# Kernel tuning notes

Measured on AMD Instinct MI355X. Metric: run time of the kernel, lower is better.

## Reference

```python
import jax, jax.numpy as jnp
import numpy as np

N = 6144
IN_F = 256
OUT_F = 64
ALPHA = 0.2  # leaky relu slope
NEG_INF = -9e15
ADJ_DENSITY = 0.01


def setup_inputs() -> dict:
    key = jax.random.key(0)
    kx, ka, kw, kat, ks, ke = jax.random.split(key, 6)
    x = jax.random.normal(kx, (N, IN_F), dtype=jnp.float32)
    adj = (jax.random.uniform(ka, (N, N)) < ADJ_DENSITY).astype(jnp.float32)
    adj = adj.at[jnp.arange(N), jnp.arange(N)].set(0.0)
    # xavier-uniform-ish init scale (gain 1.414)
    def xavier(k, shape):
        fan_in, fan_out = shape[0], shape[1]
        lim = 1.414 * np.sqrt(6.0 / (fan_in + fan_out))
        return jax.random.uniform(k, shape, minval=-lim, maxval=lim, dtype=jnp.float32)
    W = xavier(kw, (IN_F, OUT_F))
    a = xavier(kat, (2 * OUT_F, 1))
    W_si = xavier(ks, (1, 1))
    W_ei = xavier(ke, (1, 1))
    return {"x": x, "adj": adj, "W": W, "a": a, "W_si": W_si, "W_ei": W_ei}


def reference(x, adj, W, a, W_si, W_ei):
    # h: [N, F_out]
    h = x @ W
    # additive GAT score: e[i,j] = leakyrelu(Wh1[i] + Wh2[j])
    Wh1 = h @ a[:OUT_F, :]           # [N, 1]
    Wh2 = h @ a[OUT_F:, :]           # [N, 1]
    e = jax.nn.leaky_relu(Wh1 + Wh2.T, negative_slope=ALPHA)  # [N, N]
    # adjacency-power topology bias
    adj2 = adj @ adj
    adj3 = adj2 @ adj
    adj_w = adj + adj2 + adj3
    adj_w = adj_w.at[jnp.arange(N), jnp.arange(N)].set(0.0)
    e = jnp.abs(W_ei) * e + jnp.abs(W_si) * adj_w
    # masked softmax over neighbors (row-wise)
    scores = jnp.where(adj > 0, e, NEG_INF)
    attention = jax.nn.softmax(scores, axis=1)
    # dropout omitted (eval mode / training=False)
    h_prime = attention @ h
    return jax.nn.elu(h_prime)
```

## Files before the change

kernel.cpp:

```cpp
#include <hip/hip_runtime.h>
#include <math.h>

#define N 6144
#define MAXD 128
#define NWORDS 96
#define NW32 192

typedef unsigned long long u64;
typedef unsigned int u32;
typedef unsigned char u8;
typedef float f4 __attribute__((ext_vector_type(4)));


__device__ __forceinline__ int a_addr(int j) {
    int vdx = (j & ~255) | ((j & 3) << 6) | ((j >> 2) & 63);
    return (((vdx >> 2) & 7) << 10) | ((vdx >> 5) << 2) | (vdx & 3);
}

#define FA(s, c, a, b, ci) { u32 _t = (a) ^ (b); (s) = _t ^ (ci); (c) = ((a) & (b)) | ((ci) & _t); }

template <int START>
__device__ __forceinline__ void badd_from(u32* p, u32 cy) {
    #pragma unroll
    for (int q = START; q < 6; ++q) { u32 x = p[q] & cy; p[q] ^= cy; cy = x; }
    p[6] ^= cy;
}

__device__ __forceinline__ void csa15(u32* p, const u32* x) {
    u32 s0,c0,s1,c1,s2,c2,s3,c3,s4,c4;
    FA(s0,c0, x[0], x[1], x[2]);
    FA(s1,c1, x[3], x[4], x[5]);
    FA(s2,c2, x[6], x[7], x[8]);
    FA(s3,c3, x[9], x[10], x[11]);
    FA(s4,c4, x[12], x[13], x[14]);
    u32 t0,d0,u0,d1;
    FA(t0,d0, s0, s1, s2);
    FA(u0,d1, s3, s4, t0);
    u32 e0,f0,e1,f1,e2,f2;
    FA(e0,f0, c0, c1, c2);
    FA(e1,f1, c3, c4, d0);
    FA(e2,f2, e0, e1, d1);
    u32 g0,h0;
    FA(g0,h0, f0, f1, f2);
    badd_from<0>(p, u0);
    badd_from<1>(p, e2);
    badd_from<2>(p, g0);
    badd_from<3>(p, h0);
}

__global__ __launch_bounds__(256) void k_gemm_h(
    const float* __restrict__ x, const float* __restrict__ W,
    const float* __restrict__ a,
    float* __restrict__ h, float* __restrict__ Wh1, float* __restrict__ Wh2,
    int* __restrict__ col_cnt)
{
    int gid = blockIdx.x * 256 + threadIdx.x;
    if (gid < N) col_cnt[gid] = 0;

    __shared__ float Wl[256 * 64];
    int t = threadIdx.x;
    #pragma unroll
    for (int c = 0; c < 64; ++c) Wl[c * 256 + t] = W[c * 256 + t];
    __syncthreads();

    int w = t >> 6, lane = t & 63;
    int i0 = blockIdx.x * 32 + w * 8;
    const float* xr = x + (long)i0 * 256;

    float acc[8] = {0.f, 0.f, 0.f, 0.f, 0.f, 0.f, 0.f, 0.f};
    for (int k0 = 0; k0 < 256; k0 += 4) {
        float4 xv[8];
        #pragma unroll
        for (int r = 0; r < 8; ++r)
            xv[r] = *(const float4*)(xr + (long)r * 256 + k0);
        #pragma unroll
        for (int kk = 0; kk < 4; ++kk) {
            float wv = Wl[(k0 + kk) * 64 + lane];
            #pragma unroll
            for (int r = 0; r < 8; ++r) {
                float xs = (kk == 0) ? xv[r].x : (kk == 1) ? xv[r].y
                         : (kk == 2) ? xv[r].z : xv[r].w;
                acc[r] = fmaf(xs, wv, acc[r]);
            }
        }
    }

    #pragma unroll
    for (int r = 0; r < 8; ++r) {
        int i = i0 + r;
        h[(long)i * 64 + lane] = acc[r];
        float s1 = acc[r] * a[lane];
        float s2 = acc[r] * a[64 + lane];
        #pragma unroll
        for (int off = 32; off; off >>= 1) {
            s1 += __shfl_xor(s1, off, 64);
            s2 += __shfl_xor(s2, off, 64);
        }
        if (lane == 0) { Wh1[i] = s1; Wh2[i] = s2; }
    }
}

__global__ __launch_bounds__(256) void k_build(
    const float* __restrict__ adj,
    u64* __restrict__ rowbits, int* __restrict__ row_cnt, int* __restrict__ row_list,
    int* __restrict__ col_cnt, int* __restrict__ col_list)
{
    int i = blockIdx.x;
    int t = threadIdx.x, w = t >> 6, lane = t & 63;
    __shared__ int cnt;
    if (t == 0) cnt = 0;
    __syncthreads();

    const f4* ar = (const f4*)(adj + (long)i * N) + (w * 6) * 64;

    f4 v[6];
    #pragma unroll
    for (int c = 0; c < 6; ++c)
        v[c] = __builtin_nontemporal_load(ar + c * 64 + lane);

    u64 m[6][4];
    #pragma unroll
    for (int c = 0; c < 6; ++c) {
        m[c][0] = __ballot(v[c].x != 0.0f);
        m[c][1] = __ballot(v[c].y != 0.0f);
        m[c][2] = __ballot(v[c].z != 0.0f);
        m[c][3] = __ballot(v[c].w != 0.0f);
    }

    int tot = 0;
    #pragma unroll
    for (int c = 0; c < 6; ++c) {
        #pragma unroll
        for (int p = 0; p < 4; ++p) tot += __popcll(m[c][p]);
    }
    int base = 0;
    if (lane == 0 && tot) base = atomicAdd(&cnt, tot);
    base = __shfl(base, 0, 64);

    u64* rb = rowbits + (long)i * NWORDS + w * 24;
    #pragma unroll
    for (int c = 0; c < 6; ++c) {
        #pragma unroll
        for (int p = 0; p < 4; ++p) {
            u64 mm = m[c][p];
            if (lane == 0) rb[c * 4 + p] = mm;
            if ((mm >> lane) & 1ull) {
                int rank = __popcll(mm & ((1ull << lane) - 1ull));
                int s = base + rank;
                int j = (w * 6 + c) * 256 + (lane << 2) + p;
                if (s < MAXD) row_list[(long)i * MAXD + s] = j;
                int sc = atomicAdd(&col_cnt[j], 1);
                if (sc < MAXD) col_list[(long)j * MAXD + sc] = i;
            }
            base += __popcll(mm);
        }
    }
    __syncthreads();
    if (t == 0) row_cnt[i] = cnt < 127 ? cnt : 127;
}

__global__ __launch_bounds__(192) void k_attn(
    const float* __restrict__ h, const float* __restrict__ Wh1, const float* __restrict__ Wh2,
    const u64* __restrict__ rowbits,
    const int* __restrict__ row_cnt, const int* __restrict__ row_list,
    const int* __restrict__ col_cnt, const int* __restrict__ col_list,
    const float* __restrict__ W_si, const float* __restrict__ W_ei,
    float* __restrict__ out)
{
    __shared__ u32 adj2p[8 * 256];
    __shared__ int nbr[MAXD];
    __shared__ int ccbuf[MAXD];
    __shared__ float lrbuf[MAXD];
    __shared__ float ebuf[MAXD];
    __shared__ float part[192];
    __shared__ float sh_max, sh_sum;

    int i = blockIdx.x;
    int t = threadIdx.x, w = t >> 6, lane = t & 63;
    int deg = row_cnt[i];
    deg = deg < 127 ? deg : 127;

    if (deg == 0) {
        float acc = 0.f;
        for (int r = w; r < N; r += 3) acc += h[(long)r * 64 + lane];
        part[t] = acc;
        __syncthreads();
        if (w == 0) {
            float s = part[lane] + part[64 + lane] + part[128 + lane];
            s *= (1.0f / N);
            out[(long)i * 64 + lane] = s > 0.f ? s : expm1f(s);
        }
        return;
    }

    float aWei = fabsf(W_ei[0]);
    float aWsi = fabsf(W_si[0]);

    if (t < deg) {
        int j = row_list[(long)i * MAXD + t];
        nbr[t] = j;
        int cc = col_cnt[j];
        ccbuf[t] = cc < MAXD ? cc : MAXD;
        float z = Wh1[i] + Wh2[j];
        lrbuf[t] = aWei * (z > 0.f ? z : 0.2f * z);
    }

    {
        const u32* rb32 = (const u32*)rowbits;
        const int* rl = row_list + (long)i * MAXD;
        u32 p[7] = {0,0,0,0,0,0,0};

        int m = 0;
        for (; m + 15 <= deg; m += 15) {
            u32 x[15];
            #pragma unroll
            for (int q = 0; q < 15; ++q) {
                int j = rl[m + q];
                x[q] = rb32[(long)j * NW32 + t];
            }
            csa15(p, x);
        }
        if (m < deg) {
            u32 x[15];
            #pragma unroll
            for (int q = 0; q < 15; ++q) {
                int mq = m + q;
                int j = rl[mq < deg ? mq : 0];
                u32 vv = rb32[(long)j * NW32 + t];
                x[q] = (mq < deg) ? vv : 0u;
            }
            csa15(p, x);
        }

        #pragma unroll
        for (int g = 0; g < 8; ++g) {
            u32 acc = 0;
            #pragma unroll
            for (int pl = 0; pl < 7; ++pl) {
                u32 nib = (p[pl] >> (4 * g)) & 0xFu;
                acc += (nib * (0x00204081u << pl)) & (0x01010101u << pl);
            }
            adj2p[g * 256 + t] = acc;
        }
    }
    __syncthreads();

    const u8* adj2b = (const u8*)adj2p;

    {
        int g = t >> 3, sub = t & 7;
        for (int e = g; e < deg; e += 24) {
            int j = nbr[e];
            int cc = ccbuf[e];
            const int* cl = col_list + (long)j * MAXD;
            u32 a3 = 0;
            for (int q = sub; q < cc; q += 8) {
                int k = cl[q];
                a3 += (u32)adj2b[a_addr(k)];
            }
            a3 += __shfl_xor(a3, 1, 64);
            a3 += __shfl_xor(a3, 2, 64);
            a3 += __shfl_xor(a3, 4, 64);
            if (sub == 0) {
                u32 a2 = (u32)adj2b[a_addr(j)];
                ebuf[e] = lrbuf[e] + aWsi * (float)(1u + a2 + a3);
            }
        }
    }
    __syncthreads();

    if (w == 0) {
        float v = -3.4e38f;
        for (int idx = lane; idx < deg; idx += 64) v = fmaxf(v, ebuf[idx]);
        #pragma unroll
        for (int off = 32; off; off >>= 1) v = fmaxf(v, __shfl_xor(v, off, 64));
        if (lane == 0) sh_max = v;
    }
    __syncthreads();
    if (t < deg) ebuf[t] = expf(ebuf[t] - sh_max);
    __syncthreads();
    if (w == 0) {
        float s = 0.f;
        for (int idx = lane; idx < deg; idx += 64) s += ebuf[idx];
        #pragma unroll
        for (int off = 32; off; off >>= 1) s += __shfl_xor(s, off, 64);
        if (lane == 0) sh_sum = s;
    }
    __syncthreads();

    float acc0 = 0.f, acc1 = 0.f;
    int e = w;
    for (; e + 3 < deg; e += 6) {
        acc0 = fmaf(ebuf[e],     h[(long)nbr[e]     * 64 + lane], acc0);
        acc1 = fmaf(ebuf[e + 3], h[(long)nbr[e + 3] * 64 + lane], acc1);
    }
    if (e < deg)
        acc0 = fmaf(ebuf[e], h[(long)nbr[e] * 64 + lane], acc0);
    part[t] = acc0 + acc1;
    __syncthreads();
    if (w == 0) {
        float s = part[lane] + part[64 + lane] + part[128 + lane];
        s /= sh_sum;
        out[(long)i * 64 + lane] = s > 0.f ? s : expm1f(s);
    }
}

extern "C" void kernel_launch(void* const* d_in, const int* in_sizes, int n_in,
                              void* d_out, int out_size, void* d_ws, size_t ws_size,
                              hipStream_t stream) {
    const float* x    = (const float*)d_in[0];
    const float* adj  = (const float*)d_in[1];
    const float* W    = (const float*)d_in[2];
    const float* a    = (const float*)d_in[3];
    const float* W_si = (const float*)d_in[4];
    const float* W_ei = (const float*)d_in[5];
    float* out = (float*)d_out;

    char* ws = (char*)d_ws;
    size_t off = 0;
    auto alloc = [&](size_t bytes) -> void* {
        void* p = ws + off;
        off += (bytes + 255) & ~(size_t)255;
        return p;
    };
    u64*   rowbits  = (u64*)  alloc((size_t)N * NWORDS * sizeof(u64));
    float* h        = (float*)alloc((size_t)N * 64 * sizeof(float));
    float* Wh1      = (float*)alloc((size_t)N * sizeof(float));
    float* Wh2      = (float*)alloc((size_t)N * sizeof(float));
    int*   row_cnt  = (int*)  alloc((size_t)N * sizeof(int));
    int*   row_list = (int*)  alloc((size_t)N * MAXD * sizeof(int));
    int*   col_cnt  = (int*)  alloc((size_t)N * sizeof(int));
    int*   col_list = (int*)  alloc((size_t)N * MAXD * sizeof(int));

    k_gemm_h<<<N / 32, 256, 0, stream>>>(x, W, a, h, Wh1, Wh2, col_cnt);
    k_build <<<N, 256, 0, stream>>>(adj, rowbits, row_cnt, row_list, col_cnt, col_list);
    k_attn  <<<N, 192, 0, stream>>>(h, Wh1, Wh2, rowbits, row_cnt, row_list,
                                    col_cnt, col_list, W_si, W_ei, out);
}
```

Before: 325.5 us.

## Build column lists via bit-matrix transpose instead of global atomics

Removes the per-nonzero global atomicAdd on col_cnt and the scattered col_list writes from the adjacency scan. Instead the row bitmask is transposed with a warp-shuffle 64x64 bit transpose into a column bitmask, and a separate kernel builds each column list with a wave prefix scan. The per-block shared atomic for the row count is also replaced by per-wave totals in shared memory. This adds two extra kernel launches and a second 4.7MB bitmask buffer. The column list order becomes deterministic (sorted by row) rather than atomic-order.

```diff
diff --git a/kernel.cpp b/kernel.cpp
--- a/kernel.cpp
+++ b/kernel.cpp
@@ -48,15 +48,26 @@
     badd_from<3>(p, h0);
 }
 
+__device__ __forceinline__ u64 bit_transpose64(u64 x, int lane) {
+    const u64 masks[6] = {0xAAAAAAAAAAAAAAAAull, 0xCCCCCCCCCCCCCCCCull,
+                          0xF0F0F0F0F0F0F0F0ull, 0xFF00FF00FF00FF00ull,
+                          0xFFFF0000FFFF0000ull, 0xFFFFFFFF00000000ull};
+    #pragma unroll
+    for (int k = 0; k < 6; ++k) {
+        int s = 1 << k;
+        u64 m = masks[k];
+        u64 y = (u64)__shfl_xor((long long)x, s, 64);
+        x = (lane & s) ? ((x & m) | ((y & m) >> s))
+                       : ((x & ~m) | ((y & ~m) << s));
+    }
+    return x;
+}
+
 __global__ __launch_bounds__(256) void k_gemm_h(
     const float* __restrict__ x, const float* __restrict__ W,
     const float* __restrict__ a,
-    float* __restrict__ h, float* __restrict__ Wh1, float* __restrict__ Wh2,
-    int* __restrict__ col_cnt)
+    float* __restrict__ h, float* __restrict__ Wh1, float* __restrict__ Wh2)
 {
-    int gid = blockIdx.x * 256 + threadIdx.x;
-    if (gid < N) col_cnt[gid] = 0;
-
     __shared__ float Wl[256 * 64];
     int t = threadIdx.x;
     #pragma unroll
@@ -102,14 +113,11 @@
 
 __global__ __launch_bounds__(256) void k_build(
     const float* __restrict__ adj,
-    u64* __restrict__ rowbits, int* __restrict__ row_cnt, int* __restrict__ row_list,
-    int* __restrict__ col_cnt, int* __restrict__ col_list)
+    u64* __restrict__ rowbits, int* __restrict__ row_cnt, int* __restrict__ row_list)
 {
     int i = blockIdx.x;
     int t = threadIdx.x, w = t >> 6, lane = t & 63;
-    __shared__ int cnt;
-    if (t == 0) cnt = 0;
-    __syncthreads();
+    __shared__ int wtot[4];
 
     const f4* ar = (const f4*)(adj + (long)i * N) + (w * 6) * 64;
 
@@ -133,9 +141,11 @@
         #pragma unroll
         for (int p = 0; p < 4; ++p) tot += __popcll(m[c][p]);
     }
+    if (lane == 0) wtot[w] = tot;
+    __syncthreads();
     int base = 0;
-    if (lane == 0 && tot) base = atomicAdd(&cnt, tot);
-    base = __shfl(base, 0, 64);
+    #pragma unroll
+    for (int q = 0; q < 4; ++q) if (q < w) base += wtot[q];
 
     u64* rb = rowbits + (long)i * NWORDS + w * 24;
     #pragma unroll
@@ -149,14 +159,65 @@
                 int s = base + rank;
                 int j = (w * 6 + c) * 256 + (lane << 2) + p;
                 if (s < MAXD) row_list[(long)i * MAXD + s] = j;
-                int sc = atomicAdd(&col_cnt[j], 1);
-                if (sc < MAXD) col_list[(long)j * MAXD + sc] = i;
             }
             base += __popcll(mm);
         }
     }
-    __syncthreads();
-    if (t == 0) row_cnt[i] = cnt < 127 ? cnt : 127;
+    if (t == 0) {
+        int tt = wtot[0] + wtot[1] + wtot[2] + wtot[3];
+        row_cnt[i] = tt < 127 ? tt : 127;
+    }
+}
+
+__global__ __launch_bounds__(256) void k_trans(
+    const u64* __restrict__ rowbits, u64* __restrict__ colbits)
+{
+    int w = threadIdx.x >> 6, lane = threadIdx.x & 63;
+    int tile = blockIdx.x * 4 + w;
+    int tr = tile / 96, tc = tile - tr * 96;
+    u64 x = rowbits[(long)(tr * 64 + lane) * NWORDS + tc];
+    x = bit_transpose64(x, lane);
+    colbits[(long)(tc * 64 + lane) * NWORDS + tr] = x;
+}
+
+__global__ __launch_bounds__(256) void k_collist(
+    const u64* __restrict__ colbits,
+    int* __restrict__ col_cnt, int* __restrict__ col_list)
+{
+    int w = threadIdx.x >> 6, lane = threadIdx.x & 63;
+    int v = blockIdx.x * 4 + w;
+    int j = (v & ~255) | ((v & 63) << 2) | ((v >> 6) & 3);
+
+    u64 w0 = 0, w1 = 0;
+    if (lane < 48) {
+        const u64* p2 = colbits + (long)v * NWORDS + lane * 2;
+        w0 = p2[0]; w1 = p2[1];
+    }
+    int pc = __popcll(w0) + __popcll(w1);
+    int incl = pc;
+    #pragma unroll
+    for (int off = 1; off < 64; off <<= 1) {
+        int y = __shfl_up(incl, off, 64);
+        if (lane >= off) incl += y;
+    }
+    int excl = incl - pc;
+    int total = __shfl(incl, 63, 64);
+    if (lane == 0) col_cnt[j] = total;
+
+    int* cl = col_list + (long)j * MAXD;
+    int s = excl;
+    int ibase = lane * 128;
+    while (w0) {
+        int b = __ffsll((long long)w0) - 1; w0 &= w0 - 1;
+        if (s < MAXD) cl[s] = ibase + b;
+        ++s;
+    }
+    ibase += 64;
+    while (w1) {
+        int b = __ffsll((long long)w1) - 1; w1 &= w1 - 1;
+        if (s < MAXD) cl[s] = ibase + b;
+        ++s;
+    }
 }
 
 __global__ __launch_bounds__(192) void k_attn(
@@ -324,6 +385,7 @@
         return p;
     };
     u64*   rowbits  = (u64*)  alloc((size_t)N * NWORDS * sizeof(u64));
+    u64*   colbits  = (u64*)  alloc((size_t)N * NWORDS * sizeof(u64));
     float* h        = (float*)alloc((size_t)N * 64 * sizeof(float));
     float* Wh1      = (float*)alloc((size_t)N * sizeof(float));
     float* Wh2      = (float*)alloc((size_t)N * sizeof(float));
@@ -332,8 +394,10 @@
     int*   col_cnt  = (int*)  alloc((size_t)N * sizeof(int));
     int*   col_list = (int*)  alloc((size_t)N * MAXD * sizeof(int));
 
-    k_gemm_h<<<N / 32, 256, 0, stream>>>(x, W, a, h, Wh1, Wh2, col_cnt);
-    k_build <<<N, 256, 0, stream>>>(adj, rowbits, row_cnt, row_list, col_cnt, col_list);
-    k_attn  <<<N, 192, 0, stream>>>(h, Wh1, Wh2, rowbits, row_cnt, row_list,
-                                    col_cnt, col_list, W_si, W_ei, out);
-}
+    k_gemm_h <<<N / 32, 256, 0, stream>>>(x, W, a, h, Wh1, Wh2);
+    k_build  <<<N, 256, 0, stream>>>(adj, rowbits, row_cnt, row_list);
+    k_trans  <<<(96 * 96) / 4, 256, 0, stream>>>(rowbits, colbits);
+    k_collist<<<N / 4, 256, 0, stream>>>(colbits, col_cnt, col_list);
+    k_attn   <<<N, 192, 0, stream>>>(h, Wh1, Wh2, rowbits, row_cnt, row_list,
+                                     col_cnt, col_list, W_si, W_ei, out);
+}
```

Result: faster. 311.1 us (-4.4%).
